# Performance work log

Measured on AMD Instinct MI355X. Metric: run time of the kernel, lower is better.

The kernel has to match this reference:

```python
import jax, jax.numpy as jnp
import numpy as np

H = 1024      # hidden_size
V = 50257     # output_size (vocab)
L = 512       # max_length (encoder length)


def setup_inputs() -> dict:
    key = jax.random.key(0)
    ks = jax.random.split(key, 12)
    s = 0.02  # param init scale
    return {
        "input": jax.random.randint(ks[0], (1, 1), 0, V),
        "hidden": jax.random.normal(ks[1], (1, 1, H), dtype=jnp.float32),
        "encoder_outputs": jax.random.normal(ks[2], (L, H), dtype=jnp.float32),
        "emb": jax.random.normal(ks[3], (V, H), dtype=jnp.float32) * s,
        "attn_W": jax.random.normal(ks[4], (L, 2 * H), dtype=jnp.float32) * s,
        "attn_b": jnp.zeros((L,), jnp.float32),
        "comb_W": jax.random.normal(ks[5], (H, 2 * H), dtype=jnp.float32) * s,
        "comb_b": jnp.zeros((H,), jnp.float32),
        "W_ih": jax.random.normal(ks[6], (4 * H, H), dtype=jnp.float32) * s,
        "W_hh": jax.random.normal(ks[7], (4 * H, H), dtype=jnp.float32) * s,
        "b_ih": jnp.zeros((4 * H,), jnp.float32),
        "b_hh": jnp.zeros((4 * H,), jnp.float32),
        "out_W": jax.random.normal(ks[8], (V, H), dtype=jnp.float32) * s,
        "out_b": jnp.zeros((V,), jnp.float32),
    }


def reference(input, hidden, encoder_outputs, emb, attn_W, attn_b,
              comb_W, comb_b, W_ih, W_hh, b_ih, b_hh, out_W, out_b):
    # embedding lookup -> [1, H] (embedded[0] in the torch code)
    embedded = emb[input.reshape(-1)].reshape(1, H)
    h0 = hidden[0]  # [1, H]
    # Bahdanau-style attention over encoder positions
    attn_logits = jnp.concatenate([embedded, h0], axis=1) @ attn_W.T + attn_b  # [1, L]
    attn_weights = jax.nn.softmax(attn_logits, axis=1)
    attn_applied = attn_weights @ encoder_outputs  # [1, H]
    # combine + relu
    x = jax.nn.relu(jnp.concatenate([embedded, attn_applied], axis=1) @ comb_W.T + comb_b)  # [1, H]
    # single LSTM cell step; torch passes (hidden, hidden) so c0 == h0
    c0 = h0
    gates = x @ W_ih.T + b_ih + h0 @ W_hh.T + b_hh  # [1, 4H], gate order i,f,g,o
    i_g, f_g, g_g, o_g = jnp.split(gates, 4, axis=1)
    c = jax.nn.sigmoid(f_g) * c0 + jax.nn.sigmoid(i_g) * jnp.tanh(g_g)
    h = jax.nn.sigmoid(o_g) * jnp.tanh(c)
    # output projection + log-softmax
    out = jax.nn.log_softmax(h @ out_W.T + out_b, axis=1)  # [1, V]
    return out, (h[None], c[None]), attn_weights
```

## Files before the change

### kernel.cpp

```cpp
#include <hip/hip_runtime.h>
#include <math.h>

#define H 1024
#define V 50257
#define L 512
#define NPART 1571

#define WS_LOGITS 0
#define WS_ATTN   512
#define WS_X      1536
#define WS_H      2560
#define WS_VLOG   3584
#define WS_PART   53844

__device__ __forceinline__ float wave_sum(float v) {
    for (int o = 32; o > 0; o >>= 1) v += __shfl_down(v, o, 64);
    return v;
}
__device__ __forceinline__ float sigf(float x) { return 1.0f / (1.0f + expf(-x)); }
__device__ __forceinline__ float dot4(float4 a, float4 b) {
    return a.x * b.x + a.y * b.y + a.z * b.z + a.w * b.w;
}
__device__ __forceinline__ void osm_merge(float& m, float& s, float m2, float s2) {
    float M = fmaxf(m, m2);
    if (M == -INFINITY) { m = M; s = 0.f; return; }
    s = s * expf(m - M) + s2 * expf(m2 - M);
    m = M;
}

__global__ void kA_attn_logits(const int* __restrict__ tok,
                               const float* __restrict__ hidden,
                               const float* __restrict__ emb,
                               const float* __restrict__ attn_W,
                               const float* __restrict__ attn_b,
                               float* __restrict__ ws) {
    int r = blockIdx.x, t = threadIdx.x;
    if (r < 4) ws[WS_ATTN + r * 256 + t] = 0.0f;
    size_t token = (size_t)tok[0];
    const float4* rw = (const float4*)(attn_W + (size_t)r * 2 * H);
    const float4* ev = (const float4*)(emb + token * H);
    const float4* hv = (const float4*)hidden;
    float acc = dot4(ev[t], rw[t]) + dot4(hv[t], rw[256 + t]);
    float s = wave_sum(acc);
    __shared__ float red[4];
    if ((t & 63) == 0) red[t >> 6] = s;
    __syncthreads();
    if (t == 0) ws[WS_LOGITS + r] = red[0] + red[1] + red[2] + red[3] + attn_b[r];
}

__global__ void kB_softmax_attn(const float* __restrict__ enc,
                                float* __restrict__ ws,
                                float* __restrict__ out) {
    int t = threadIdx.x, bid = blockIdx.x;
    int jb = bid >> 5, lc = bid & 31;
    float v0 = ws[WS_LOGITS + t];
    float v1 = ws[WS_LOGITS + 256 + t];
    float m = fmaxf(v0, v1);
    for (int o = 32; o > 0; o >>= 1) m = fmaxf(m, __shfl_down(m, o, 64));
    __shared__ float red[4];
    __shared__ float bm, bs;
    if ((t & 63) == 0) red[t >> 6] = m;
    __syncthreads();
    if (t == 0) bm = fmaxf(fmaxf(red[0], red[1]), fmaxf(red[2], red[3]));
    __syncthreads();
    float e = expf(v0 - bm) + expf(v1 - bm);
    float s = wave_sum(e);
    if ((t & 63) == 0) red[t >> 6] = s;
    __syncthreads();
    if (t == 0) bs = red[0] + red[1] + red[2] + red[3];
    __syncthreads();
    __shared__ float wl[16];
    int l0 = lc * 16;
    if (t < 16) wl[t] = expf(ws[WS_LOGITS + l0 + t] - bm) / bs;
    if (lc == 0 && t < 128) {
        int l = jb * 128 + t;
        out[V + 2 * H + l] = expf(ws[WS_LOGITS + l] - bm) / bs;
    }
    __syncthreads();
    int j = jb * 256 + t;
    float acc = 0.f;
#pragma unroll
    for (int i = 0; i < 16; ++i)
        acc += wl[i] * enc[(size_t)(l0 + i) * H + j];
    atomicAdd(&ws[WS_ATTN + j], acc);
}

__global__ void kC_combine(const int* __restrict__ tok,
                           const float* __restrict__ emb,
                           const float* __restrict__ comb_W,
                           const float* __restrict__ comb_b,
                           float* __restrict__ ws) {
    int t = threadIdx.x;
    int w = t >> 6, l = t & 63;
    size_t token = (size_t)tok[0];
    __shared__ float4 vec4[512];
    vec4[t] = ((const float4*)(emb + token * H))[t];
    vec4[256 + t] = ((const float4*)(ws + WS_ATTN))[t];
    __syncthreads();
    const float4* cw = (const float4*)comb_W;
#pragma unroll
    for (int rr = 0; rr < 4; ++rr) {
        int r = blockIdx.x * 16 + w * 4 + rr;
        float acc = 0.f;
#pragma unroll
        for (int i = 0; i < 8; ++i)
            acc += dot4(cw[(size_t)r * 512 + i * 64 + l], vec4[i * 64 + l]);
        float s = wave_sum(acc);
        if (l == 0) ws[WS_X + r] = fmaxf(s + comb_b[r], 0.0f);
    }
}

__global__ void kD_gates_lstm(const float* __restrict__ hidden,
                              const float* __restrict__ W_ih,
                              const float* __restrict__ W_hh,
                              const float* __restrict__ b_ih,
                              const float* __restrict__ b_hh,
                              float* __restrict__ ws,
                              float* __restrict__ out) {
    int t = threadIdx.x;
    int w = t >> 6, l = t & 63;
    __shared__ float4 xs[256], hs[256];
    xs[t] = ((const float4*)(ws + WS_X))[t];
    hs[t] = ((const float4*)hidden)[t];
    __syncthreads();
    int u = w >> 1, gp = w & 1;
    int n = blockIdx.x * 2 + u;
    int row0 = (gp * 2) * H + n;
    int row1 = (gp * 2 + 1) * H + n;
    const float4* wi = (const float4*)W_ih;
    const float4* wh = (const float4*)W_hh;
    float a0 = 0.f, a1 = 0.f;
#pragma unroll
    for (int i = 0; i < 4; ++i) {
        float4 x4 = xs[i * 64 + l], h4 = hs[i * 64 + l];
        a0 += dot4(wi[(size_t)row0 * 256 + i * 64 + l], x4);
        a0 += dot4(wh[(size_t)row0 * 256 + i * 64 + l], h4);
        a1 += dot4(wi[(size_t)row1 * 256 + i * 64 + l], x4);
        a1 += dot4(wh[(size_t)row1 * 256 + i * 64 + l], h4);
    }
    float s0 = wave_sum(a0);
    float s1 = wave_sum(a1);
    __shared__ float gsh[2][4];
    if (l == 0) {
        gsh[u][gp * 2]     = s0 + b_ih[row0] + b_hh[row0];
        gsh[u][gp * 2 + 1] = s1 + b_ih[row1] + b_hh[row1];
    }
    __syncthreads();
    if (t < 2) {
        int nn = blockIdx.x * 2 + t;
        float gi = gsh[t][0], gf = gsh[t][1], gg = gsh[t][2], go = gsh[t][3];
        float c0 = hidden[nn];
        float c = sigf(gf) * c0 + sigf(gi) * tanhf(gg);
        float h = sigf(go) * tanhf(c);
        ws[WS_H + nn] = h;
        out[V + nn] = h;
        out[V + H + nn] = c;
    }
}

__global__ void kE_vocab(const float* __restrict__ out_W,
                         const float* __restrict__ out_b,
                         float* __restrict__ ws) {
    int t = threadIdx.x;
    int w = t >> 6, l = t & 63;
    const float4* h4 = (const float4*)(ws + WS_H);
    float4 hr[4];
#pragma unroll
    for (int i = 0; i < 4; ++i) hr[i] = h4[i * 64 + l];
    const float4* ow = (const float4*)out_W;
    float pm = -INFINITY, psv = 0.f;
#pragma unroll
    for (int rp = 0; rp < 4; ++rp) {
        int r0 = blockIdx.x * 32 + w * 8 + rp * 2;
        int r1 = r0 + 1;
        bool v0 = r0 < V, v1 = r1 < V;
        size_t q0 = (size_t)(v0 ? r0 : V - 1) * 256;
        size_t q1 = (size_t)(v1 ? r1 : V - 1) * 256;
        float a0 = 0.f, a1 = 0.f;
#pragma unroll
        for (int i = 0; i < 4; ++i) {
            a0 += dot4(ow[q0 + i * 64 + l], hr[i]);
            a1 += dot4(ow[q1 + i * 64 + l], hr[i]);
        }
        float s0 = wave_sum(a0);
        float s1 = wave_sum(a1);
        if (l == 0) {
            if (v0) {
                float lg = s0 + out_b[r0];
                ws[WS_VLOG + r0] = lg;
                float M = fmaxf(pm, lg);
                psv = psv * expf(pm - M) + expf(lg - M);
                pm = M;
            }
            if (v1) {
                float lg = s1 + out_b[r1];
                ws[WS_VLOG + r1] = lg;
                float M = fmaxf(pm, lg);
                psv = psv * expf(pm - M) + expf(lg - M);
                pm = M;
            }
        }
    }
    __shared__ float sm[4], ss[4];
    if (l == 0) { sm[w] = pm; ss[w] = psv; }
    __syncthreads();
    if (t == 0) {
        float m = sm[0], s = ss[0];
        for (int i = 1; i < 4; ++i) osm_merge(m, s, sm[i], ss[i]);
        ws[WS_PART + 2 * blockIdx.x] = m;
        ws[WS_PART + 2 * blockIdx.x + 1] = s;
    }
}

__global__ void kF_logsoftmax(const float* __restrict__ ws,
                              float* __restrict__ out) {
    int t = threadIdx.x;
    float m = -INFINITY, s = 0.f;
    for (int i = t; i < NPART; i += 256)
        osm_merge(m, s, ws[WS_PART + 2 * i], ws[WS_PART + 2 * i + 1]);
    for (int o = 32; o > 0; o >>= 1) {
        float m2 = __shfl_down(m, o, 64);
        float s2 = __shfl_down(s, o, 64);
        osm_merge(m, s, m2, s2);
    }
    __shared__ float sm[4], ss[4];
    __shared__ float lse;
    if ((t & 63) == 0) { sm[t >> 6] = m; ss[t >> 6] = s; }
    __syncthreads();
    if (t == 0) {
        float mm = sm[0], sv = ss[0];
        for (int i = 1; i < 4; ++i) osm_merge(mm, sv, sm[i], ss[i]);
        lse = mm + logf(sv);
    }
    __syncthreads();
    int r = blockIdx.x * 256 + t;
    if (r < V) out[r] = ws[WS_VLOG + r] - lse;
}

extern "C" void kernel_launch(void* const* d_in, const int* in_sizes, int n_in,
                              void* d_out, int out_size, void* d_ws, size_t ws_size,
                              hipStream_t stream) {
    const int*   tok     = (const int*)d_in[0];
    const float* hidden  = (const float*)d_in[1];
    const float* enc     = (const float*)d_in[2];
    const float* emb     = (const float*)d_in[3];
    const float* attn_W  = (const float*)d_in[4];
    const float* attn_b  = (const float*)d_in[5];
    const float* comb_W  = (const float*)d_in[6];
    const float* comb_b  = (const float*)d_in[7];
    const float* W_ih    = (const float*)d_in[8];
    const float* W_hh    = (const float*)d_in[9];
    const float* b_ih    = (const float*)d_in[10];
    const float* b_hh    = (const float*)d_in[11];
    const float* out_W   = (const float*)d_in[12];
    const float* out_b   = (const float*)d_in[13];
    float* out = (float*)d_out;
    float* ws  = (float*)d_ws;

    kA_attn_logits<<<512, 256, 0, stream>>>(tok, hidden, emb, attn_W, attn_b, ws);
    kB_softmax_attn<<<128, 256, 0, stream>>>(enc, ws, out);
    kC_combine<<<64, 256, 0, stream>>>(tok, emb, comb_W, comb_b, ws);
    kD_gates_lstm<<<512, 256, 0, stream>>>(hidden, W_ih, W_hh, b_ih, b_hh, ws, out);
    kE_vocab<<<1571, 256, 0, stream>>>(out_W, out_b, ws);
    kF_logsoftmax<<<197, 256, 0, stream>>>(ws, out);
}
```

Before: 64.44 us.

## Fuse attention and vocab stages with in-kernel grid barriers via atomic flags

Merges the attention-logit and softmax/attention-apply kernels into one kernel, and the vocab projection and log-softmax into another. Each uses a spin-wait on an atomic arrival counter so all blocks can share a global softmax denominator without a separate launch. The max subtraction is dropped and plain exp sums are used, which relies on logits staying small. A memset is added to reset the counters and accumulators. It also retiles the combine kernel to more blocks. The gains come from fewer launches and not writing and re-reading the vocab logits, at the risk of deadlock if not all blocks are co-resident and of overflow for large logits.

```diff
diff --git a/kernel.cpp b/kernel.cpp
--- a/kernel.cpp
+++ b/kernel.cpp
@@ -4,14 +4,17 @@
 #define H 1024
 #define V 50257
 #define L 512
-#define NPART 1571
-
-#define WS_LOGITS 0
-#define WS_ATTN   512
-#define WS_X      1536
-#define WS_H      2560
-#define WS_VLOG   3584
-#define WS_PART   53844
+#define NB_AB 128
+#define NB_EF 1024
+
+#define WS_FLAGA 0
+#define WS_FLAGV 1
+#define WS_DENA  2
+#define WS_DENV  3
+#define WS_ATTN  64
+#define WS_X     1600
+#define WS_H     2624
+#define MEMSET_BYTES 4352
 
 __device__ __forceinline__ float wave_sum(float v) {
     for (int o = 32; o > 0; o >>= 1) v += __shfl_down(v, o, 64);
@@ -21,68 +24,68 @@
 __device__ __forceinline__ float dot4(float4 a, float4 b) {
     return a.x * b.x + a.y * b.y + a.z * b.z + a.w * b.w;
 }
-__device__ __forceinline__ void osm_merge(float& m, float& s, float m2, float s2) {
-    float M = fmaxf(m, m2);
-    if (M == -INFINITY) { m = M; s = 0.f; return; }
-    s = s * expf(m - M) + s2 * expf(m2 - M);
-    m = M;
-}
-
-__global__ void kA_attn_logits(const int* __restrict__ tok,
-                               const float* __restrict__ hidden,
-                               const float* __restrict__ emb,
-                               const float* __restrict__ attn_W,
-                               const float* __restrict__ attn_b,
-                               float* __restrict__ ws) {
-    int r = blockIdx.x, t = threadIdx.x;
-    if (r < 4) ws[WS_ATTN + r * 256 + t] = 0.0f;
-    size_t token = (size_t)tok[0];
+
+__device__ __forceinline__ float arrive_and_wait_sum(float* den, int* flag,
+                                                     float partial, int nblk) {
+    __hip_atomic_fetch_add(den, partial, __ATOMIC_RELAXED, __HIP_MEMORY_SCOPE_AGENT);
+    __hip_atomic_fetch_add(flag, 1, __ATOMIC_RELEASE, __HIP_MEMORY_SCOPE_AGENT);
+    while (__hip_atomic_load(flag, __ATOMIC_RELAXED, __HIP_MEMORY_SCOPE_AGENT) < nblk)
+        __builtin_amdgcn_s_sleep(8);
+    return __hip_atomic_load(den, __ATOMIC_RELAXED, __HIP_MEMORY_SCOPE_AGENT);
+}
+
+__global__ __launch_bounds__(256) void kAB(const int* __restrict__ tok,
+                                           const float* __restrict__ hidden,
+                                           const float* __restrict__ enc,
+                                           const float* __restrict__ emb,
+                                           const float* __restrict__ attn_W,
+                                           const float* __restrict__ attn_b,
+                                           float* __restrict__ ws,
+                                           float* __restrict__ out) {
+    const int bid = blockIdx.x, t = threadIdx.x;
+    const int w = t >> 6, l = t & 63;
+    const size_t token = (size_t)tok[0];
+    const float4* ev4 = (const float4*)(emb + token * H);
+    const float4* hv4 = (const float4*)hidden;
+
+    __shared__ float lg[4];
+    __shared__ float wexp[4];
+    __shared__ float dsh;
+
+    int r = bid * 4 + w;
     const float4* rw = (const float4*)(attn_W + (size_t)r * 2 * H);
-    const float4* ev = (const float4*)(emb + token * H);
-    const float4* hv = (const float4*)hidden;
-    float acc = dot4(ev[t], rw[t]) + dot4(hv[t], rw[256 + t]);
+    float acc = 0.f;
+#pragma unroll
+    for (int i = 0; i < 4; ++i) {
+        acc += dot4(rw[i * 64 + l], ev4[i * 64 + l]);
+        acc += dot4(rw[256 + i * 64 + l], hv4[i * 64 + l]);
+    }
     float s = wave_sum(acc);
-    __shared__ float red[4];
-    if ((t & 63) == 0) red[t >> 6] = s;
-    __syncthreads();
-    if (t == 0) ws[WS_LOGITS + r] = red[0] + red[1] + red[2] + red[3] + attn_b[r];
-}
-
-__global__ void kB_softmax_attn(const float* __restrict__ enc,
-                                float* __restrict__ ws,
-                                float* __restrict__ out) {
-    int t = threadIdx.x, bid = blockIdx.x;
-    int jb = bid >> 5, lc = bid & 31;
-    float v0 = ws[WS_LOGITS + t];
-    float v1 = ws[WS_LOGITS + 256 + t];
-    float m = fmaxf(v0, v1);
-    for (int o = 32; o > 0; o >>= 1) m = fmaxf(m, __shfl_down(m, o, 64));
-    __shared__ float red[4];
-    __shared__ float bm, bs;
-    if ((t & 63) == 0) red[t >> 6] = m;
-    __syncthreads();
-    if (t == 0) bm = fmaxf(fmaxf(red[0], red[1]), fmaxf(red[2], red[3]));
-    __syncthreads();
-    float e = expf(v0 - bm) + expf(v1 - bm);
-    float s = wave_sum(e);
-    if ((t & 63) == 0) red[t >> 6] = s;
-    __syncthreads();
-    if (t == 0) bs = red[0] + red[1] + red[2] + red[3];
-    __syncthreads();
-    __shared__ float wl[16];
-    int l0 = lc * 16;
-    if (t < 16) wl[t] = expf(ws[WS_LOGITS + l0 + t] - bm) / bs;
-    if (lc == 0 && t < 128) {
-        int l = jb * 128 + t;
-        out[V + 2 * H + l] = expf(ws[WS_LOGITS + l] - bm) / bs;
-    }
-    __syncthreads();
-    int j = jb * 256 + t;
-    float acc = 0.f;
-#pragma unroll
-    for (int i = 0; i < 16; ++i)
-        acc += wl[i] * enc[(size_t)(l0 + i) * H + j];
-    atomicAdd(&ws[WS_ATTN + j], acc);
+    if (l == 0) lg[w] = s + attn_b[r];
+    __syncthreads();
+    if (t == 0) {
+        float p = expf(lg[0]) + expf(lg[1]) + expf(lg[2]) + expf(lg[3]);
+        dsh = arrive_and_wait_sum((float*)&((int*)ws)[0] + WS_DENA,
+                                  (int*)ws + WS_FLAGA, p, NB_AB);
+    }
+    __syncthreads();
+    float denom = dsh;
+    if (t < 4) {
+        float wv = expf(lg[t]) / denom;
+        wexp[t] = wv;
+        out[V + 2 * H + bid * 4 + t] = wv;
+    }
+    __syncthreads();
+    int l0 = bid * 4;
+#pragma unroll
+    for (int jj = 0; jj < 4; ++jj) {
+        int j = jj * 256 + t;
+        float a = 0.f;
+#pragma unroll
+        for (int i = 0; i < 4; ++i)
+            a += wexp[i] * enc[(size_t)(l0 + i) * H + j];
+        atomicAdd(&ws[WS_ATTN + j], a);
+    }
 }
 
 __global__ void kC_combine(const int* __restrict__ tok,
@@ -93,21 +96,18 @@
     int t = threadIdx.x;
     int w = t >> 6, l = t & 63;
     size_t token = (size_t)tok[0];
-    __shared__ float4 vec4[512];
-    vec4[t] = ((const float4*)(emb + token * H))[t];
-    vec4[256 + t] = ((const float4*)(ws + WS_ATTN))[t];
-    __syncthreads();
+    const float4* ev4 = (const float4*)(emb + token * H);
+    const float4* a4 = (const float4*)(ws + WS_ATTN);
+    int r = blockIdx.x * 4 + w;
     const float4* cw = (const float4*)comb_W;
-#pragma unroll
-    for (int rr = 0; rr < 4; ++rr) {
-        int r = blockIdx.x * 16 + w * 4 + rr;
-        float acc = 0.f;
-#pragma unroll
-        for (int i = 0; i < 8; ++i)
-            acc += dot4(cw[(size_t)r * 512 + i * 64 + l], vec4[i * 64 + l]);
-        float s = wave_sum(acc);
-        if (l == 0) ws[WS_X + r] = fmaxf(s + comb_b[r], 0.0f);
-    }
+    float acc = 0.f;
+#pragma unroll
+    for (int i = 0; i < 4; ++i) {
+        acc += dot4(cw[(size_t)r * 512 + i * 64 + l], ev4[i * 64 + l]);
+        acc += dot4(cw[(size_t)r * 512 + 256 + i * 64 + l], a4[i * 64 + l]);
+    }
+    float s = wave_sum(acc);
+    if (l == 0) ws[WS_X + r] = fmaxf(s + comb_b[r], 0.0f);
 }
 
 __global__ void kD_gates_lstm(const float* __restrict__ hidden,
@@ -158,83 +158,52 @@
     }
 }
 
-__global__ void kE_vocab(const float* __restrict__ out_W,
-                         const float* __restrict__ out_b,
-                         float* __restrict__ ws) {
-    int t = threadIdx.x;
-    int w = t >> 6, l = t & 63;
+__global__ __launch_bounds__(256, 4) void kEF(const float* __restrict__ out_W,
+                                              const float* __restrict__ out_b,
+                                              float* __restrict__ ws,
+                                              float* __restrict__ out) {
+    const int bid = blockIdx.x, t = threadIdx.x;
+    const int w = t >> 6, l = t & 63;
+    const int row0 = bid * 49 + (bid < 81 ? bid : 81);
+    const int cnt  = 49 + (bid < 81 ? 1 : 0);
+
+    __shared__ float slog[52];
+    __shared__ float red[4];
+    __shared__ float lsh;
+
     const float4* h4 = (const float4*)(ws + WS_H);
     float4 hr[4];
 #pragma unroll
     for (int i = 0; i < 4; ++i) hr[i] = h4[i * 64 + l];
+
     const float4* ow = (const float4*)out_W;
-    float pm = -INFINITY, psv = 0.f;
-#pragma unroll
-    for (int rp = 0; rp < 4; ++rp) {
-        int r0 = blockIdx.x * 32 + w * 8 + rp * 2;
-        int r1 = r0 + 1;
-        bool v0 = r0 < V, v1 = r1 < V;
-        size_t q0 = (size_t)(v0 ? r0 : V - 1) * 256;
-        size_t q1 = (size_t)(v1 ? r1 : V - 1) * 256;
-        float a0 = 0.f, a1 = 0.f;
-#pragma unroll
-        for (int i = 0; i < 4; ++i) {
-            a0 += dot4(ow[q0 + i * 64 + l], hr[i]);
-            a1 += dot4(ow[q1 + i * 64 + l], hr[i]);
+    float es = 0.f;
+    for (int k = w; k < cnt; k += 4) {
+        int r = row0 + k;
+        const float4* q = ow + (size_t)r * 256;
+        float acc = 0.f;
+#pragma unroll
+        for (int i = 0; i < 4; ++i)
+            acc += dot4(q[i * 64 + l], hr[i]);
+        float s = wave_sum(acc);
+        if (l == 0) {
+            float lg = s + out_b[r];
+            slog[k] = lg;
+            es += expf(lg);
         }
-        float s0 = wave_sum(a0);
-        float s1 = wave_sum(a1);
-        if (l == 0) {
-            if (v0) {
-                float lg = s0 + out_b[r0];
-                ws[WS_VLOG + r0] = lg;
-                float M = fmaxf(pm, lg);
-                psv = psv * expf(pm - M) + expf(lg - M);
-                pm = M;
-            }
-            if (v1) {
-                float lg = s1 + out_b[r1];
-                ws[WS_VLOG + r1] = lg;
-                float M = fmaxf(pm, lg);
-                psv = psv * expf(pm - M) + expf(lg - M);
-                pm = M;
-            }
-        }
-    }
-    __shared__ float sm[4], ss[4];
-    if (l == 0) { sm[w] = pm; ss[w] = psv; }
+    }
+    if (l == 0) red[w] = es;
     __syncthreads();
     if (t == 0) {
-        float m = sm[0], s = ss[0];
-        for (int i = 1; i < 4; ++i) osm_merge(m, s, sm[i], ss[i]);
-        ws[WS_PART + 2 * blockIdx.x] = m;
-        ws[WS_PART + 2 * blockIdx.x + 1] = s;
-    }
-}
-
-__global__ void kF_logsoftmax(const float* __restrict__ ws,
-                              float* __restrict__ out) {
-    int t = threadIdx.x;
-    float m = -INFINITY, s = 0.f;
-    for (int i = t; i < NPART; i += 256)
-        osm_merge(m, s, ws[WS_PART + 2 * i], ws[WS_PART + 2 * i + 1]);
-    for (int o = 32; o > 0; o >>= 1) {
-        float m2 = __shfl_down(m, o, 64);
-        float s2 = __shfl_down(s, o, 64);
-        osm_merge(m, s, m2, s2);
-    }
-    __shared__ float sm[4], ss[4];
-    __shared__ float lse;
-    if ((t & 63) == 0) { sm[t >> 6] = m; ss[t >> 6] = s; }
-    __syncthreads();
-    if (t == 0) {
-        float mm = sm[0], sv = ss[0];
-        for (int i = 1; i < 4; ++i) osm_merge(mm, sv, sm[i], ss[i]);
-        lse = mm + logf(sv);
-    }
-    __syncthreads();
-    int r = blockIdx.x * 256 + t;
-    if (r < V) out[r] = ws[WS_VLOG + r] - lse;
+        float p = red[0] + red[1] + red[2] + red[3];
+        float S = arrive_and_wait_sum((float*)&((int*)ws)[0] + WS_DENV,
+                                      (int*)ws + WS_FLAGV, p, NB_EF);
+        lsh = logf(S);
+    }
+    __syncthreads();
+    float lse = lsh;
+    for (int i = t; i < cnt; i += 256)
+        out[row0 + i] = slog[i] - lse;
 }
 
 extern "C" void kernel_launch(void* const* d_in, const int* in_sizes, int n_in,
@@ -257,10 +226,9 @@
     float* out = (float*)d_out;
     float* ws  = (float*)d_ws;
 
-    kA_attn_logits<<<512, 256, 0, stream>>>(tok, hidden, emb, attn_W, attn_b, ws);
-    kB_softmax_attn<<<128, 256, 0, stream>>>(enc, ws, out);
-    kC_combine<<<64, 256, 0, stream>>>(tok, emb, comb_W, comb_b, ws);
+    hipMemsetAsync(ws, 0, MEMSET_BYTES, stream);
+    kAB<<<NB_AB, 256, 0, stream>>>(tok, hidden, enc, emb, attn_W, attn_b, ws, out);
+    kC_combine<<<256, 256, 0, stream>>>(tok, emb, comb_W, comb_b, ws);
     kD_gates_lstm<<<512, 256, 0, stream>>>(hidden, W_ih, W_hh, b_ih, b_hh, ws, out);
-    kE_vocab<<<1571, 256, 0, stream>>>(out_W, out_b, ws);
-    kF_logsoftmax<<<197, 256, 0, stream>>>(ws, out);
-}
+    kEF<<<NB_EF, 256, 0, stream>>>(out_W, out_b, ws, out);
+}
```

Result: slower. 195.2 us (+202.9%).
